# Kernel optimization log

Hardware: AMD Instinct MI355X
Metric: run time of the kernel (lower is better)

The kernel has to match this reference:

```python
import jax, jax.numpy as jnp
import numpy as np

B, NPER, F, D, E, NUM_STEPS = 256, 512, 256, 32, 524288, 4
N = B * NPER
INIT_TAU, TAU_SCALE, STEP_ALPHA = 0.1, 0.5, 5.0


def setup_inputs() -> dict:
    key = jax.random.key(0)
    ks = jax.random.split(key, 10)
    x_start = jax.random.uniform(ks[0], (N,), jnp.float32, 0.1, 1.0)   # strictly positive iterate
    x_solution = jax.random.uniform(ks[1], (N,), jnp.float32, 0.0, 1.0)
    q = jax.random.normal(ks[2], (N,), jnp.float32)
    edge_src = jax.random.randint(ks[3], (E,), 0, N, jnp.int32)
    edge_dst = jax.random.randint(ks[4], (E,), 0, N, jnp.int32)
    vals_batch = jnp.repeat(jnp.arange(B, dtype=jnp.int32), NPER)      # equal-sized graphs
    proj_matrix = jax.random.normal(ks[5], (B, NPER, F), jnp.float32) / np.float32(np.sqrt(NPER))
    W_in = jax.random.normal(ks[6], (2, D), jnp.float32) / np.float32(np.sqrt(2.0))
    b_in = jnp.zeros((D,), jnp.float32)
    W_msg = jax.random.normal(ks[7], (D, D), jnp.float32) / np.float32(np.sqrt(D))
    b_msg = jnp.zeros((D,), jnp.float32)
    W_out = jax.random.normal(ks[8], (D, 1), jnp.float32) / np.float32(np.sqrt(D))
    b_out = jnp.zeros((1,), jnp.float32)
    return {"x_start": x_start, "x_solution": x_solution, "q": q,
            "proj_matrix": proj_matrix, "W_in": W_in, "b_in": b_in,
            "W_msg": W_msg, "b_msg": b_msg, "W_out": W_out, "b_out": b_out,
            "edge_src": edge_src, "edge_dst": edge_dst, "vals_batch": vals_batch}


def _l1_normalize(x, batch):
    # per-graph L1 normalization: x / sum_i |x_i| over the graph segment
    s = jax.ops.segment_sum(jnp.abs(x), batch, num_segments=B)
    return x / (s[batch] + 1e-12)


def _line_search(x, d, batch, max_alpha):
    # largest per-graph alpha s.t. x + alpha*d >= 0, capped at max_alpha
    ratio = jnp.where(d < 0, x / jnp.maximum(-d, 1e-12), max_alpha)
    a = jnp.clip(jax.ops.segment_min(ratio, batch, num_segments=B), 0.0, max_alpha)
    return a[batch]  # gathered back to per-node


def _gnn(xs, q, edge_src, edge_dst, W_in, b_in, W_msg, b_msg, W_out, b_out):
    h = jax.nn.relu(jnp.stack([xs, q], axis=-1) @ W_in + b_in)      # [N, D]
    m = h[edge_src] @ W_msg + b_msg                                  # [E, D]
    agg = jax.ops.segment_sum(m, edge_dst, num_segments=N)          # [N, D]
    h2 = jax.nn.relu(h + agg)
    return h2 @ W_out[:, 0] + b_out[0]                               # [N]


def reference(x_start, x_solution, q, proj_matrix, W_in, b_in, W_msg, b_msg,
              W_out, b_out, edge_src, edge_dst, vals_batch):
    tau = INIT_TAU
    xs = x_start
    preds, labels = [], []
    for _ in range(NUM_STEPS):
        pred = _gnn(xs, q, edge_src, edge_dst, W_in, b_in, W_msg, b_msg, W_out, b_out)
        preds.append(pred)
        labels.append(_l1_normalize(x_solution - xs, vals_batch))
        p = _l1_normalize(jax.lax.stop_gradient(pred), vals_batch)   # .detach() in torch
        direction = p + 3.0 * tau / (xs + tau)
        tau = max(tau * TAU_SCALE, 1e-5)
        # to_dense_batch with equal graph sizes == reshape; project onto nullspace basis
        dd = direction.reshape(B, NPER)
        df = jnp.einsum('bnf,bn->bf', proj_matrix, dd)               # [B, F]
        pproj = jnp.einsum('bnf,bf->bn', proj_matrix, df).reshape(-1)  # [N]
        alpha = _line_search(xs, pproj, vals_batch, STEP_ALPHA) * 0.995
        xs = xs + alpha * pproj
    return jnp.stack(preds, axis=1), jnp.stack(labels, axis=1)       # each [N, NUM_STEPS]
```

## Files before the change

### kernel.cpp

```cpp
#include <hip/hip_runtime.h>

#define BB 256
#define NPER 512
#define FF 256
#define DD 32
#define EE 524288
#define NN (BB*NPER)
#define NSTEPS 4

__device__ __forceinline__ float bflo(unsigned u) { return __uint_as_float(u << 16); }
__device__ __forceinline__ float bfhi(unsigned u) { return __uint_as_float(u & 0xFFFF0000u); }
__device__ __forceinline__ unsigned rtn_bf16(unsigned u) {
    return (u + 0x7FFFu + ((u >> 16) & 1u)) >> 16;
}


__global__ void k_degpack(const int* __restrict__ dst, unsigned* __restrict__ deg,
                          const float* __restrict__ xs0, const float* __restrict__ q,
                          float2* __restrict__ xq) {
    int t = blockIdx.x * blockDim.x + threadIdx.x;
    if (t < NN) { float2 v; v.x = xs0[t]; v.y = q[t]; xq[t] = v; }
    atomicAdd(&deg[dst[t]], 1u);
}

__global__ __launch_bounds__(256) void k_alloc(const unsigned* __restrict__ deg,
                                               unsigned* __restrict__ gcur,
                                               unsigned* __restrict__ rowstart,
                                               unsigned* __restrict__ cursor) {
    __shared__ unsigned r[256];
    __shared__ unsigned base;
    int t = threadIdx.x;
    int i = blockIdx.x * 256 + t;
    unsigned d = deg[i];
    r[t] = d;
    __syncthreads();
    for (int o = 1; o < 256; o <<= 1) {
        unsigned v = (t >= o) ? r[t - o] : 0u;
        __syncthreads();
        r[t] += v;
        __syncthreads();
    }
    if (t == 255) base = atomicAdd(gcur, r[255]);
    __syncthreads();
    unsigned excl = r[t] - d + base;
    rowstart[i] = excl;
    cursor[i] = excl;
}

__global__ void k_fill(const int* __restrict__ src, const int* __restrict__ dst,
                       unsigned* __restrict__ cursor, int* __restrict__ csr_src) {
    int e = blockIdx.x * blockDim.x + threadIdx.x;
    unsigned pos = atomicAdd(&cursor[dst[e]], 1u);
    csr_src[pos] = src[e];
}


template<int STEP>
__global__ void k_node_g(const float2* __restrict__ xq,
                         const float* __restrict__ Win, const float* __restrict__ bin,
                         const unsigned* __restrict__ rowstart, const unsigned* __restrict__ deg,
                         const int* __restrict__ csr_src,
                         const float* __restrict__ Wmsg, const float* __restrict__ bmsg,
                         const float* __restrict__ Wout, const float* __restrict__ bout,
                         float* __restrict__ pred, float* __restrict__ out_preds) {
    int tid = threadIdx.x;
    int d = tid & 31;
    int i = blockIdx.x * 8 + (tid >> 5);
    float w0 = Win[d], w1 = Win[DD + d], b0 = bin[d];
    float wcol[DD];
    #pragma unroll
    for (int k = 0; k < DD; ++k) wcol[k] = Wmsg[k * DD + d];
    unsigned rs = rowstart[i];
    unsigned dg = deg[i];
    unsigned nfull = dg < 32u ? dg : 32u;
    float xv = 0.f, qv = 0.f;
    if ((unsigned)d < nfull) {
        int sv = csr_src[rs + d];
        float2 v = xq[sv];
        xv = v.x; qv = v.y;
    }
    float s = 0.f;
    for (unsigned j = 0; j < nfull; ++j) {
        float xj = __shfl(xv, (int)j, 32);
        float qj = __shfl(qv, (int)j, 32);
        s += fmaxf(xj * w0 + qj * w1 + b0, 0.f);
    }
    for (unsigned j = 32; j < dg; ++j) {
        int sv = csr_src[rs + j];
        float2 v = xq[sv];
        s += fmaxf(v.x * w0 + v.y * w1 + b0, 0.f);
    }
    float2 self = xq[i];
    float hval = fmaxf(self.x * w0 + self.y * w1 + b0, 0.f);
    float agg = (float)dg * bmsg[d];
    #pragma unroll
    for (int k = 0; k < DD; ++k) agg += __shfl(s, k, 32) * wcol[k];
    float h2 = fmaxf(hval + agg, 0.f);
    float v = h2 * Wout[d];
    for (int o = 16; o > 0; o >>= 1) v += __shfl_down(v, o, 32);
    if (d == 0) {
        float pr = v + bout[0];
        pred[i] = pr;
        out_preds[i * NSTEPS + STEP] = pr;
    }
}

template<int STEP0>
__global__ __launch_bounds__(1024) void k_stepR(const float* __restrict__ Pf,
                                                unsigned short* __restrict__ Pbf,
                                                float2* __restrict__ xq,
                                                const float* __restrict__ xsol,
                                                const float* __restrict__ pred,
                                                float* __restrict__ out_labels,
                                                float tau, int step, int last) {
    __shared__ float dd_l[NPER], x_l[NPER], pp_l[NPER];
    __shared__ float sl[16 * FF];
    __shared__ float dfl[FF];
    __shared__ float redA[16], redB[16], wmin[16];
    int b = blockIdx.x;
    int t = threadIdx.x;
    int w = t >> 6, lane = t & 63;
    int gbase = b * NPER;

    float x = 0.f, r = 0.f, p = 0.f, a1 = 0.f, a2 = 0.f;
    if (t < NPER) {
        x = xq[gbase + t].x;
        r = xsol[gbase + t] - x;
        p = pred[gbase + t];
        a1 = fabsf(r); a2 = fabsf(p);
    }
    #pragma unroll
    for (int o = 32; o > 0; o >>= 1) {
        a1 += __shfl_down(a1, o, 64);
        a2 += __shfl_down(a2, o, 64);
    }
    if (lane == 0) { redA[w] = a1; redB[w] = a2; }
    __syncthreads();
    float Sr = 1e-12f, Sp = 1e-12f;
    #pragma unroll
    for (int k = 0; k < 16; ++k) { Sr += redA[k]; Sp += redB[k]; }
    if (t < NPER) {
        out_labels[(size_t)(gbase + t) * NSTEPS + step] = r / Sr;
        x_l[t] = x;
        dd_l[t] = p / Sp + 3.0f * tau / (x + tau);
    }
    __syncthreads();

    size_t pbase = ((size_t)(gbase + w * 32)) * FF + 4 * lane;
    unsigned pl[64];
    float4 acc = {0.f, 0.f, 0.f, 0.f};
    if (STEP0) {
        const float4* Pr = (const float4*)(Pf + pbase);
        uint2* Pw = (uint2*)(Pbf + pbase);
        #pragma unroll
        for (int n = 0; n < 32; ++n) {
            float4 pv = Pr[(size_t)n * 64];
            float sc = dd_l[w * 32 + n];
            acc.x += pv.x * sc; acc.y += pv.y * sc;
            acc.z += pv.z * sc; acc.w += pv.w * sc;
            unsigned u0 = rtn_bf16(__float_as_uint(pv.x));
            unsigned u1 = rtn_bf16(__float_as_uint(pv.y));
            unsigned u2 = rtn_bf16(__float_as_uint(pv.z));
            unsigned u3 = rtn_bf16(__float_as_uint(pv.w));
            unsigned lo = u0 | (u1 << 16), hi = u2 | (u3 << 16);
            uint2 o2; o2.x = lo; o2.y = hi;
            Pw[(size_t)n * 64] = o2;
            pl[2 * n] = lo; pl[2 * n + 1] = hi;
        }
    } else {
        const uint2* Pr = (const uint2*)(Pbf + pbase);
        #pragma unroll
        for (int n = 0; n < 32; ++n) {
            uint2 pv = Pr[(size_t)n * 64];
            float sc = dd_l[w * 32 + n];
            acc.x += bflo(pv.x) * sc; acc.y += bfhi(pv.x) * sc;
            acc.z += bflo(pv.y) * sc; acc.w += bfhi(pv.y) * sc;
            pl[2 * n] = pv.x; pl[2 * n + 1] = pv.y;
        }
    }
    ((float4*)sl)[w * 64 + lane] = acc;
    __syncthreads();
    if (t < FF) {
        float v = 0.f;
        #pragma unroll
        for (int k = 0; k < 16; ++k) v += sl[k * FF + t];
        dfl[t] = v;
    }
    __syncthreads();

    float4 dfv = ((const float4*)dfl)[lane];
    float mloc = 5.0f;
    #pragma unroll
    for (int n = 0; n < 32; ++n) {
        float pr = bflo(pl[2 * n]) * dfv.x + bfhi(pl[2 * n]) * dfv.y
                 + bflo(pl[2 * n + 1]) * dfv.z + bfhi(pl[2 * n + 1]) * dfv.w;
        #pragma unroll
        for (int o = 1; o < 64; o <<= 1) pr += __shfl_xor(pr, o, 64);
        if (lane == 0) pp_l[w * 32 + n] = pr;
        float xr = x_l[w * 32 + n];
        float ratio = (pr < 0.f) ? (xr / fmaxf(-pr, 1e-12f)) : 5.0f;
        mloc = fminf(mloc, ratio);
    }
    if (lane == 0) wmin[w] = mloc;
    __syncthreads();

    float mm = wmin[0];
    #pragma unroll
    for (int k = 1; k < 16; ++k) mm = fminf(mm, wmin[k]);
    float alpha = fminf(fmaxf(mm, 0.f), 5.0f) * 0.995f;
    float xnew = 0.f;
    if (t < NPER) {
        xnew = x_l[t] + alpha * pp_l[t];
        xq[gbase + t].x = xnew;
    }
    if (last) {
        float rr = 0.f, aa = 0.f;
        if (t < NPER) { rr = xsol[gbase + t] - xnew; aa = fabsf(rr); }
        #pragma unroll
        for (int o = 32; o > 0; o >>= 1) aa += __shfl_down(aa, o, 64);
        __syncthreads();
        if (lane == 0) redA[w] = aa;
        __syncthreads();
        float Sr2 = 1e-12f;
        #pragma unroll
        for (int k = 0; k < 16; ++k) Sr2 += redA[k];
        if (t < NPER) out_labels[(size_t)(gbase + t) * NSTEPS + (NSTEPS - 1)] = rr / Sr2;
    }
}


extern "C" void kernel_launch(void* const* d_in, const int* in_sizes, int n_in,
                              void* d_out, int out_size, void* d_ws, size_t ws_size,
                              hipStream_t stream) {
    const float* x_start = (const float*)d_in[0];
    const float* x_sol   = (const float*)d_in[1];
    const float* q       = (const float*)d_in[2];
    const float* P       = (const float*)d_in[3];
    const float* Win     = (const float*)d_in[4];
    const float* bin     = (const float*)d_in[5];
    const float* Wmsg    = (const float*)d_in[6];
    const float* bmsg    = (const float*)d_in[7];
    const float* Wout    = (const float*)d_in[8];
    const float* bout    = (const float*)d_in[9];
    const int*   esrc    = (const int*)d_in[10];
    const int*   edst    = (const int*)d_in[11];

    float* out_preds  = (float*)d_out;
    float* out_labels = (float*)d_out + (size_t)NN * NSTEPS;

    float* w = (float*)d_ws;
    unsigned* deg  = (unsigned*)w; w += NN;
    unsigned* gcur = (unsigned*)w; w += 2;
    float2* xq  = (float2*)w; w += 2 * (size_t)NN;
    float* pred  = w; w += NN;
    unsigned* rowstart = (unsigned*)w; w += NN;
    unsigned* cursor   = (unsigned*)w; w += NN;
    int* csr_src       = (int*)w;      w += EE;
    unsigned short* Pbf = (unsigned short*)w;

    hipMemsetAsync(deg, 0, (NN + 2) * sizeof(unsigned), stream);
    k_degpack<<<EE / 256, 256, 0, stream>>>(edst, deg, x_start, q, xq);
    k_alloc<<<NN / 256, 256, 0, stream>>>(deg, gcur, rowstart, cursor);
    k_fill<<<EE / 256, 256, 0, stream>>>(esrc, edst, cursor, csr_src);

    float tau = 0.1f;
    for (int step = 0; step < NSTEPS; ++step) {
        switch (step) {
        case 0: k_node_g<0><<<NN / 8, 256, 0, stream>>>(xq, Win, bin, rowstart, deg, csr_src,
                                                        Wmsg, bmsg, Wout, bout, pred, out_preds); break;
        case 1: k_node_g<1><<<NN / 8, 256, 0, stream>>>(xq, Win, bin, rowstart, deg, csr_src,
                                                        Wmsg, bmsg, Wout, bout, pred, out_preds); break;
        case 2: k_node_g<2><<<NN / 8, 256, 0, stream>>>(xq, Win, bin, rowstart, deg, csr_src,
                                                        Wmsg, bmsg, Wout, bout, pred, out_preds); break;
        default: k_node_g<3><<<NN / 8, 256, 0, stream>>>(xq, Win, bin, rowstart, deg, csr_src,
                                                         Wmsg, bmsg, Wout, bout, pred, out_preds); break;
        }
        if (step < NSTEPS - 1) {
            int last = (step == NSTEPS - 2) ? 1 : 0;
            if (step == 0)
                k_stepR<1><<<BB, 1024, 0, stream>>>(P, Pbf, xq, x_sol, pred,
                                                    out_labels, tau, step, last);
            else
                k_stepR<0><<<BB, 1024, 0, stream>>>(P, Pbf, xq, x_sol, pred,
                                                    out_labels, tau, step, last);
        }
        tau = fmaxf(tau * 0.5f, 1e-5f);
    }
}
```

Before: 552.0 us.

## Drop register-cached projection tile and reload bf16 P for back-projection

The step kernel no longer keeps the 64-register copy of its bf16 projection slice (pl[64]) alive across the reduction barrier. The back-projection instead re-reads the bf16 matrix from global memory with 16-byte loads, using half-wave groups that each produce one output row through a 32-lane shuffle reduction. The per-node line-search minimum is then computed by one thread per node with a wave-level min. Both loops are also batched into groups of independent loads. This cuts register pressure for the 1024-thread blocks and reduces the number of shuffle reductions, at the cost of a second read of the bf16 matrix (likely served partly from L2).

```diff
diff --git a/kernel.cpp b/kernel.cpp
--- a/kernel.cpp
+++ b/kernel.cpp
@@ -106,7 +106,7 @@
 }
 
 template<int STEP0>
-__global__ __launch_bounds__(1024) void k_stepR(const float* __restrict__ Pf,
+__global__ __launch_bounds__(1024) void k_stepF(const float* __restrict__ Pf,
                                                 unsigned short* __restrict__ Pbf,
                                                 float2* __restrict__ xq,
                                                 const float* __restrict__ xsol,
@@ -116,7 +116,7 @@
     __shared__ float dd_l[NPER], x_l[NPER], pp_l[NPER];
     __shared__ float sl[16 * FF];
     __shared__ float dfl[FF];
-    __shared__ float redA[16], redB[16], wmin[16];
+    __shared__ float redA[16], redB[16];
     int b = blockIdx.x;
     int t = threadIdx.x;
     int w = t >> 6, lane = t & 63;
@@ -147,35 +147,42 @@
     __syncthreads();
 
     size_t pbase = ((size_t)(gbase + w * 32)) * FF + 4 * lane;
-    unsigned pl[64];
     float4 acc = {0.f, 0.f, 0.f, 0.f};
     if (STEP0) {
         const float4* Pr = (const float4*)(Pf + pbase);
         uint2* Pw = (uint2*)(Pbf + pbase);
         #pragma unroll
-        for (int n = 0; n < 32; ++n) {
-            float4 pv = Pr[(size_t)n * 64];
-            float sc = dd_l[w * 32 + n];
-            acc.x += pv.x * sc; acc.y += pv.y * sc;
-            acc.z += pv.z * sc; acc.w += pv.w * sc;
-            unsigned u0 = rtn_bf16(__float_as_uint(pv.x));
-            unsigned u1 = rtn_bf16(__float_as_uint(pv.y));
-            unsigned u2 = rtn_bf16(__float_as_uint(pv.z));
-            unsigned u3 = rtn_bf16(__float_as_uint(pv.w));
-            unsigned lo = u0 | (u1 << 16), hi = u2 | (u3 << 16);
-            uint2 o2; o2.x = lo; o2.y = hi;
-            Pw[(size_t)n * 64] = o2;
-            pl[2 * n] = lo; pl[2 * n + 1] = hi;
+        for (int nb = 0; nb < 4; ++nb) {
+            float4 pv[8];
+            #pragma unroll
+            for (int k = 0; k < 8; ++k) pv[k] = Pr[(size_t)(nb * 8 + k) * 64];
+            #pragma unroll
+            for (int k = 0; k < 8; ++k) {
+                int n = nb * 8 + k;
+                float sc = dd_l[w * 32 + n];
+                acc.x += pv[k].x * sc; acc.y += pv[k].y * sc;
+                acc.z += pv[k].z * sc; acc.w += pv[k].w * sc;
+                unsigned u0 = rtn_bf16(__float_as_uint(pv[k].x));
+                unsigned u1 = rtn_bf16(__float_as_uint(pv[k].y));
+                unsigned u2 = rtn_bf16(__float_as_uint(pv[k].z));
+                unsigned u3 = rtn_bf16(__float_as_uint(pv[k].w));
+                uint2 o2; o2.x = u0 | (u1 << 16); o2.y = u2 | (u3 << 16);
+                Pw[(size_t)n * 64] = o2;
+            }
         }
     } else {
         const uint2* Pr = (const uint2*)(Pbf + pbase);
         #pragma unroll
-        for (int n = 0; n < 32; ++n) {
-            uint2 pv = Pr[(size_t)n * 64];
-            float sc = dd_l[w * 32 + n];
-            acc.x += bflo(pv.x) * sc; acc.y += bfhi(pv.x) * sc;
-            acc.z += bflo(pv.y) * sc; acc.w += bfhi(pv.y) * sc;
-            pl[2 * n] = pv.x; pl[2 * n + 1] = pv.y;
+        for (int nb = 0; nb < 4; ++nb) {
+            uint2 pv[8];
+            #pragma unroll
+            for (int k = 0; k < 8; ++k) pv[k] = Pr[(size_t)(nb * 8 + k) * 64];
+            #pragma unroll
+            for (int k = 0; k < 8; ++k) {
+                float sc = dd_l[w * 32 + nb * 8 + k];
+                acc.x += bflo(pv[k].x) * sc; acc.y += bfhi(pv[k].x) * sc;
+                acc.z += bflo(pv[k].y) * sc; acc.w += bfhi(pv[k].y) * sc;
+            }
         }
     }
     ((float4*)sl)[w * 64 + lane] = acc;
@@ -188,29 +195,46 @@
     }
     __syncthreads();
 
-    float4 dfv = ((const float4*)dfl)[lane];
-    float mloc = 5.0f;
-    #pragma unroll
-    for (int n = 0; n < 32; ++n) {
-        float pr = bflo(pl[2 * n]) * dfv.x + bfhi(pl[2 * n]) * dfv.y
-                 + bflo(pl[2 * n + 1]) * dfv.z + bfhi(pl[2 * n + 1]) * dfv.w;
-        #pragma unroll
-        for (int o = 1; o < 64; o <<= 1) pr += __shfl_xor(pr, o, 64);
-        if (lane == 0) pp_l[w * 32 + n] = pr;
-        float xr = x_l[w * 32 + n];
-        float ratio = (pr < 0.f) ? (xr / fmaxf(-pr, 1e-12f)) : 5.0f;
-        mloc = fminf(mloc, ratio);
-    }
-    if (lane == 0) wmin[w] = mloc;
-    __syncthreads();
-
-    float mm = wmin[0];
-    #pragma unroll
-    for (int k = 1; k < 16; ++k) mm = fminf(mm, wmin[k]);
+    {
+        int g = t >> 5, l5 = t & 31;
+        float4 dfa = ((const float4*)dfl)[l5 * 2];
+        float4 dfb4 = ((const float4*)dfl)[l5 * 2 + 1];
+        const uint4* Pr4 = (const uint4*)(Pbf + (size_t)(gbase + g * 16) * FF) + l5;
+        #pragma unroll
+        for (int nb = 0; nb < 4; ++nb) {
+            uint4 pv[4];
+            #pragma unroll
+            for (int k = 0; k < 4; ++k) pv[k] = Pr4[(size_t)(nb * 4 + k) * 32];
+            #pragma unroll
+            for (int k = 0; k < 4; ++k) {
+                float a = bflo(pv[k].x) * dfa.x + bfhi(pv[k].x) * dfa.y
+                        + bflo(pv[k].y) * dfa.z + bfhi(pv[k].y) * dfa.w
+                        + bflo(pv[k].z) * dfb4.x + bfhi(pv[k].z) * dfb4.y
+                        + bflo(pv[k].w) * dfb4.z + bfhi(pv[k].w) * dfb4.w;
+                #pragma unroll
+                for (int o = 16; o > 0; o >>= 1) a += __shfl_down(a, o, 32);
+                if (l5 == 0) pp_l[g * 16 + nb * 4 + k] = a;
+            }
+        }
+    }
+    __syncthreads();
+
+    float d = 0.f, m = 5.0f;
+    if (t < NPER) {
+        d = pp_l[t];
+        m = (d < 0.f) ? (x_l[t] / fmaxf(-d, 1e-12f)) : 5.0f;
+    }
+    #pragma unroll
+    for (int o = 32; o > 0; o >>= 1) m = fminf(m, __shfl_down(m, o, 64));
+    if (lane == 0) redA[w] = m;
+    __syncthreads();
+    float mm = redA[0];
+    #pragma unroll
+    for (int k = 1; k < 16; ++k) mm = fminf(mm, redA[k]);
     float alpha = fminf(fmaxf(mm, 0.f), 5.0f) * 0.995f;
     float xnew = 0.f;
     if (t < NPER) {
-        xnew = x_l[t] + alpha * pp_l[t];
+        xnew = x_l[t] + alpha * d;
         xq[gbase + t].x = xnew;
     }
     if (last) {
@@ -219,11 +243,11 @@
         #pragma unroll
         for (int o = 32; o > 0; o >>= 1) aa += __shfl_down(aa, o, 64);
         __syncthreads();
-        if (lane == 0) redA[w] = aa;
+        if (lane == 0) redB[w] = aa;
         __syncthreads();
         float Sr2 = 1e-12f;
         #pragma unroll
-        for (int k = 0; k < 16; ++k) Sr2 += redA[k];
+        for (int k = 0; k < 16; ++k) Sr2 += redB[k];
         if (t < NPER) out_labels[(size_t)(gbase + t) * NSTEPS + (NSTEPS - 1)] = rr / Sr2;
     }
 }
@@ -278,10 +302,10 @@
         if (step < NSTEPS - 1) {
             int last = (step == NSTEPS - 2) ? 1 : 0;
             if (step == 0)
-                k_stepR<1><<<BB, 1024, 0, stream>>>(P, Pbf, xq, x_sol, pred,
+                k_stepF<1><<<BB, 1024, 0, stream>>>(P, Pbf, xq, x_sol, pred,
                                                     out_labels, tau, step, last);
             else
-                k_stepR<0><<<BB, 1024, 0, stream>>>(P, Pbf, xq, x_sol, pred,
+                k_stepF<0><<<BB, 1024, 0, stream>>>(P, Pbf, xq, x_sol, pred,
                                                     out_labels, tau, step, last);
         }
         tau = fmaxf(tau * 0.5f, 1e-5f);
```

Measured after the change: 500.5 us. 1.1x faster.
